# Kernel optimization log

Hardware: AMD Instinct MI355X
Metric: run time of the kernel (lower is better)

## Reference

```python
import jax, jax.numpy as jnp
import numpy as np
import math

B, QLEN, DMODEL, NHEAD, SKV = 16, 1, 2048, 32, 4096
HEAD_DIM = DMODEL // NHEAD  # 64


def setup_inputs() -> dict:
    key = jax.random.key(0)
    ks = jax.random.split(key, 12)
    x = jax.random.normal(ks[0], (B, QLEN, DMODEL), dtype=jnp.float32)
    last_pos = jax.random.randint(ks[1], (B,), 0, SKV, dtype=jnp.int64)
    # mask: attend to cache positions <= last_pos (broadcast over heads and q)
    mask = (jnp.arange(SKV)[None, :] <= last_pos[:, None]).reshape(B, 1, 1, SKV)
    s = 1.0 / math.sqrt(DMODEL)
    Wq = jax.random.normal(ks[2], (DMODEL, DMODEL), dtype=jnp.float32) * s
    bq = jax.random.normal(ks[3], (DMODEL,), dtype=jnp.float32) * 0.02
    Wk = jax.random.normal(ks[4], (DMODEL, DMODEL), dtype=jnp.float32) * s
    bk = jax.random.normal(ks[5], (DMODEL,), dtype=jnp.float32) * 0.02
    Wv = jax.random.normal(ks[6], (DMODEL, DMODEL), dtype=jnp.float32) * s
    bv = jax.random.normal(ks[7], (DMODEL,), dtype=jnp.float32) * 0.02
    Wo = jax.random.normal(ks[8], (DMODEL, DMODEL), dtype=jnp.float32) * s
    bo = jax.random.normal(ks[9], (DMODEL,), dtype=jnp.float32) * 0.02
    # prefilled KV cache (float32, as in the module)
    cache_k = jax.random.normal(ks[10], (B, NHEAD, SKV, HEAD_DIM), dtype=jnp.float32)
    cache_v = jax.random.normal(ks[11], (B, NHEAD, SKV, HEAD_DIM), dtype=jnp.float32)
    return {"x": x, "last_pos": last_pos, "mask": mask, "Wq": Wq, "bq": bq,
            "Wk": Wk, "bk": bk, "Wv": Wv, "bv": bv, "Wo": Wo, "bo": bo,
            "cache_k": cache_k, "cache_v": cache_v}


def reference(x, last_pos, mask, Wq, bq, Wk, bk, Wv, bv, Wo, bo, cache_k, cache_v):
    bsz, seq_len, _ = x.shape  # decode path: seq_len == 1
    # QKV projections -> [B, H, S, D]
    q = (x @ Wq + bq).reshape(bsz, seq_len, NHEAD, HEAD_DIM).transpose(0, 2, 1, 3)
    k = (x @ Wk + bk).reshape(bsz, seq_len, NHEAD, HEAD_DIM).transpose(0, 2, 1, 3)
    v = (x @ Wv + bv).reshape(bsz, seq_len, NHEAD, HEAD_DIM).transpose(0, 2, 1, 3)
    # KV-cache scatter update at last_pos (seq_len == 1 branch of the original)
    bidx = jnp.arange(bsz)
    updated_kcache = cache_k.at[bidx, :, last_pos, :].set(k[:, :, 0, :].astype(jnp.float32))
    updated_vcache = cache_v.at[bidx, :, last_pos, :].set(v[:, :, 0, :].astype(jnp.float32))
    kf = updated_kcache.astype(q.dtype)
    vf = updated_vcache.astype(q.dtype)
    # scores: [B, H, Q, SKV]
    scores = jnp.einsum("bhqd,bhkd->bhqk", q, kf) / math.sqrt(HEAD_DIM)
    scores = jnp.where(mask, scores, jnp.finfo(scores.dtype).min)
    probs = jax.nn.softmax(scores.astype(jnp.float32), axis=-1).astype(q.dtype)
    out = jnp.einsum("bhqk,bhkd->bhqd", probs, vf)
    out = out.transpose(0, 2, 1, 3).reshape(bsz, seq_len, -1)
    out = out @ Wo + bo
    return out, updated_kcache, updated_vcache
```

## Files before the change

### kernel.cpp

```cpp
#include <hip/hip_runtime.h>
#include <math.h>

#define BB 16
#define DMODEL 2048
#define NHEAD 32
#define SKV 4096
#define HDIM 64
#define BH (BB*NHEAD)
#define NSTRIP 16

typedef float f4 __attribute__((ext_vector_type(4)));

__global__ __launch_bounds__(256) void gemm_part(
    const float* __restrict__ src,
    const float* __restrict__ Wa, const float* __restrict__ Wb,
    const float* __restrict__ Wc,
    float* __restrict__ pa, float* __restrict__ pb, float* __restrict__ pc) {
  const float* W = (blockIdx.z == 0) ? Wa : ((blockIdx.z == 1) ? Wb : Wc);
  float* part    = (blockIdx.z == 0) ? pa : ((blockIdx.z == 1) ? pb : pc);
  __shared__ float xs[16][64];
  int tid = threadIdx.x;
  int i0 = blockIdx.y * 64;
  int o  = blockIdx.x * 1024 + tid * 4;
  {
    int t = tid * 4;
    int b = t >> 6, i = t & 63;
    *(f4*)&xs[b][i] = *(const f4*)&src[b * DMODEL + i0 + i];
  }
  __syncthreads();
  f4 acc[16];
#pragma unroll
  for (int b = 0; b < 16; ++b) acc[b] = (f4)0.f;
#pragma unroll 8
  for (int i = 0; i < 64; ++i) {
    f4 w = *(const f4*)&W[(size_t)(i0 + i) * DMODEL + o];
#pragma unroll
    for (int b = 0; b < 16; ++b) acc[b] += xs[b][i] * w;
  }
  float* p = part + (size_t)blockIdx.y * (16 * DMODEL) + o;
#pragma unroll
  for (int b = 0; b < 16; ++b) *(f4*)&p[b * DMODEL] = acc[b];
}

__global__ __launch_bounds__(256) void gemm_reduce(
    const float* __restrict__ pa, const float* __restrict__ pb,
    const float* __restrict__ pc,
    const float* __restrict__ ba, const float* __restrict__ bb,
    const float* __restrict__ bc,
    float* __restrict__ da, float* __restrict__ db, float* __restrict__ dc) {
  const float* p    = (blockIdx.y == 0) ? pa : ((blockIdx.y == 1) ? pb : pc);
  const float* bias = (blockIdx.y == 0) ? ba : ((blockIdx.y == 1) ? bb : bc);
  float* dst        = (blockIdx.y == 0) ? da : ((blockIdx.y == 1) ? db : dc);
  int idx = blockIdx.x * 256 + threadIdx.x;
  float s = bias[idx & (DMODEL - 1)];
#pragma unroll 8
  for (int t = 0; t < 32; ++t) s += p[(size_t)t * (16 * DMODEL) + idx];
  dst[idx] = s;
}

__global__ __launch_bounds__(256) void k_copy_scores(
    const float* __restrict__ cacheK, const float* __restrict__ knew,
    const float* __restrict__ qv, const int* __restrict__ last_pos,
    float* __restrict__ outK, float* __restrict__ scores,
    float* __restrict__ pstat) {
  int bh = blockIdx.x >> 4;
  int blk = blockIdx.x & 15;
  int j0 = blk << 8;
  int b = bh >> 5;
  int lp = last_pos[b];
  int tid = threadIdx.x;
  int wave = tid >> 6, lane = tid & 63, q4 = lane >> 4, l16 = lane & 15;
  int rbase = wave * 4 + q4;
  const f4 qf = ((const f4*)(qv + bh * HDIM))[l16];
  const f4 kn = ((const f4*)(knew + bh * HDIM))[l16];
  size_t base = ((size_t)bh * SKV + j0 + rbase) * 16 + l16;
  const f4* K4 = (const f4*)cacheK + base;
  f4* O4 = (f4*)outK + base;
  float* s = scores + (size_t)bh * SKV;
  float fv[16];
#pragma unroll
  for (int t = 0; t < 16; ++t) {
    int j = j0 + rbase + t * 16;
    f4 kv = __builtin_nontemporal_load(&K4[t * 256]);
    if (j == lp) kv = kn;
    __builtin_nontemporal_store(kv, &O4[t * 256]);
    float p = qf.x * kv.x + qf.y * kv.y + qf.z * kv.z + qf.w * kv.w;
    p += __shfl_xor(p, 1);
    p += __shfl_xor(p, 2);
    p += __shfl_xor(p, 4);
    p += __shfl_xor(p, 8);
    p *= 0.125f;
    bool valid = (j <= lp);
    if (l16 == 0 && valid) s[j] = p;
    fv[t] = valid ? p : -1e30f;
  }
  float m = fv[0];
#pragma unroll
  for (int t = 1; t < 16; ++t) m = fmaxf(m, fv[t]);
  m = fmaxf(m, __shfl_xor(m, 16));
  m = fmaxf(m, __shfl_xor(m, 32));
  float se = 0.f;
#pragma unroll
  for (int t = 0; t < 16; ++t) se += __expf(fv[t] - m);
  se += __shfl_xor(se, 16);
  se += __shfl_xor(se, 32);
  __shared__ float lm[4], ls[4];
  if (lane == 0) { lm[wave] = m; ls[wave] = se; }
  __syncthreads();
  if (tid == 0) {
    float M = fmaxf(fmaxf(lm[0], lm[1]), fmaxf(lm[2], lm[3]));
    float S = ls[0] * __expf(lm[0] - M) + ls[1] * __expf(lm[1] - M)
            + ls[2] * __expf(lm[2] - M) + ls[3] * __expf(lm[3] - M);
    pstat[(bh * 16 + blk) * 2 + 0] = M;
    pstat[(bh * 16 + blk) * 2 + 1] = S;
  }
}

__global__ __launch_bounds__(256) void v_copy_pv(
    const float* __restrict__ cacheV, const float* __restrict__ vnew,
    const float* __restrict__ scores, const float* __restrict__ pstat,
    const int* __restrict__ last_pos,
    float* __restrict__ outV, float* __restrict__ prec) {
  __shared__ float sm[16], ss[16], sp[256];
  __shared__ float part[4][64];
  int bh = blockIdx.x >> 4;
  int blk = blockIdx.x & 15;
  int j0 = blk << 8;
  int b = bh >> 5;
  int lp = last_pos[b];
  int tid = threadIdx.x;
  if (tid < 16) {
    sm[tid] = pstat[(bh * 16 + tid) * 2 + 0];
    ss[tid] = pstat[(bh * 16 + tid) * 2 + 1];
  }
  __syncthreads();
  float M = sm[0];
#pragma unroll
  for (int i = 1; i < 16; ++i) M = fmaxf(M, sm[i]);
  float S = 0.f;
#pragma unroll
  for (int i = 0; i < 16; ++i) S += ss[i] * __expf(sm[i] - M);
  float inv = 1.f / S;
  int jj = j0 + tid;
  sp[tid] = (jj <= lp) ? __expf(scores[(size_t)bh * SKV + jj] - M) * inv : 0.f;
  __syncthreads();

  int wave = tid >> 6, lane = tid & 63, q4 = lane >> 4, l16 = lane & 15;
  int rbase = wave * 4 + q4;
  const f4 vn = ((const f4*)(vnew + bh * HDIM))[l16];
  size_t base = ((size_t)bh * SKV + j0 + rbase) * 16 + l16;
  const f4* V4 = (const f4*)cacheV + base;
  f4* O4 = (f4*)outV + base;
  f4 acc = (f4)0.f;
#pragma unroll
  for (int t = 0; t < 16; ++t) {
    int j = j0 + rbase + t * 16;
    f4 vv = __builtin_nontemporal_load(&V4[t * 256]);
    if (j == lp) vv = vn;
    __builtin_nontemporal_store(vv, &O4[t * 256]);
    acc += sp[rbase + t * 16] * vv;
  }
  acc.x += __shfl_xor(acc.x, 16); acc.x += __shfl_xor(acc.x, 32);
  acc.y += __shfl_xor(acc.y, 16); acc.y += __shfl_xor(acc.y, 32);
  acc.z += __shfl_xor(acc.z, 16); acc.z += __shfl_xor(acc.z, 32);
  acc.w += __shfl_xor(acc.w, 16); acc.w += __shfl_xor(acc.w, 32);
  if (q4 == 0) ((f4*)part[wave])[l16] = acc;
  __syncthreads();
  if (tid < 64) {
    prec[(size_t)blockIdx.x * HDIM + tid] =
        part[0][tid] + part[1][tid] + part[2][tid] + part[3][tid];
  }
}

__global__ __launch_bounds__(256) void attn_gemm_part(
    const float* __restrict__ prec, const float* __restrict__ Wo,
    float* __restrict__ po) {
  __shared__ float xs[16][64];
  int tid = threadIdx.x;
  int h = blockIdx.y;
  {
    int g = tid >> 4, u = tid & 15;
    const float* r = prec + (size_t)(g * NHEAD + h) * NSTRIP * HDIM + u * 4;
    f4 a = (f4)0.f;
#pragma unroll
    for (int s = 0; s < 16; ++s) a += *(const f4*)&r[s * HDIM];
    *(f4*)&xs[g][u * 4] = a;
  }
  __syncthreads();
  int o = blockIdx.x * 1024 + tid * 4;
  int i0 = h * 64;
  f4 acc[16];
#pragma unroll
  for (int b = 0; b < 16; ++b) acc[b] = (f4)0.f;
#pragma unroll 8
  for (int i = 0; i < 64; ++i) {
    f4 w = *(const f4*)&Wo[(size_t)(i0 + i) * DMODEL + o];
#pragma unroll
    for (int b = 0; b < 16; ++b) acc[b] += xs[b][i] * w;
  }
  float* p = po + (size_t)blockIdx.y * (16 * DMODEL) + o;
#pragma unroll
  for (int b = 0; b < 16; ++b) *(f4*)&p[b * DMODEL] = acc[b];
}

extern "C" void kernel_launch(void* const* d_in, const int* in_sizes, int n_in,
                              void* d_out, int out_size, void* d_ws, size_t ws_size,
                              hipStream_t stream) {
  const float* x        = (const float*)d_in[0];
  const int*   last_pos = (const int*)d_in[1];
  const float* Wq = (const float*)d_in[3];
  const float* bq = (const float*)d_in[4];
  const float* Wk = (const float*)d_in[5];
  const float* bk = (const float*)d_in[6];
  const float* Wv = (const float*)d_in[7];
  const float* bv = (const float*)d_in[8];
  const float* Wo = (const float*)d_in[9];
  const float* bo = (const float*)d_in[10];
  const float* cacheK = (const float*)d_in[11];
  const float* cacheV = (const float*)d_in[12];

  float* out  = (float*)d_out;
  float* outK = out + (size_t)BB * DMODEL;
  float* outV = outK + (size_t)BH * SKV * HDIM;

  float* ws    = (float*)d_ws;
  float* q     = ws;
  float* k     = ws + 32768;
  float* v     = ws + 65536;
  float* pstat = ws + 98304;
  float* prec  = ws + 114688;
  float* big   = ws + 114688 + 524288;
  float* pq = big;
  float* pk = big + 1048576;
  float* pv = big + 2097152;
  float* scores = big;
  float* po = big + 1048576;

  gemm_part<<<dim3(2, 32, 3), 256, 0, stream>>>(x, Wq, Wk, Wv, pq, pk, pv);
  gemm_reduce<<<dim3(128, 3), 256, 0, stream>>>(pq, pk, pv, bq, bk, bv, q, k, v);
  k_copy_scores<<<8192, 256, 0, stream>>>(cacheK, k, q, last_pos, outK, scores, pstat);
  v_copy_pv<<<8192, 256, 0, stream>>>(cacheV, v, scores, pstat, last_pos, outV, prec);
  attn_gemm_part<<<dim3(2, 32), 256, 0, stream>>>(prec, Wo, po);
  gemm_reduce<<<dim3(128, 1), 256, 0, stream>>>(po, po, po, bo, bo, bo, out, out, out);
}
```

Before: 441.4 us.

## Store block-local exp scores and prefetch V before softmax stats in PV kernel

The score kernel now computes the block max first and writes unnormalized exponentials relative to that max, so the PV kernel no longer recomputes exp per element. The PV kernel issues all sixteen V-cache loads up front, before reading the stats and scores, so the memory latency overlaps with the softmax-combine work. Normalization is applied once per block through a scalar rescale factor. This adds an extra block barrier in the score kernel and more live registers in the PV kernel.

```diff
diff --git a/kernel.cpp b/kernel.cpp
--- a/kernel.cpp
+++ b/kernel.cpp
@@ -89,30 +89,31 @@
     p += __shfl_xor(p, 2);
     p += __shfl_xor(p, 4);
     p += __shfl_xor(p, 8);
-    p *= 0.125f;
-    bool valid = (j <= lp);
-    if (l16 == 0 && valid) s[j] = p;
-    fv[t] = valid ? p : -1e30f;
+    fv[t] = (j <= lp) ? p * 0.125f : -1e30f;
   }
   float m = fv[0];
 #pragma unroll
   for (int t = 1; t < 16; ++t) m = fmaxf(m, fv[t]);
   m = fmaxf(m, __shfl_xor(m, 16));
   m = fmaxf(m, __shfl_xor(m, 32));
+  __shared__ float lm[4], ls[4];
+  if (lane == 0) lm[wave] = m;
+  __syncthreads();
+  float M = fmaxf(fmaxf(lm[0], lm[1]), fmaxf(lm[2], lm[3]));
   float se = 0.f;
 #pragma unroll
-  for (int t = 0; t < 16; ++t) se += __expf(fv[t] - m);
+  for (int t = 0; t < 16; ++t) {
+    float e = __expf(fv[t] - M);
+    se += e;
+    if (l16 == 0) s[j0 + rbase + t * 16] = e;
+  }
   se += __shfl_xor(se, 16);
   se += __shfl_xor(se, 32);
-  __shared__ float lm[4], ls[4];
-  if (lane == 0) { lm[wave] = m; ls[wave] = se; }
+  if (lane == 0) ls[wave] = se;
   __syncthreads();
   if (tid == 0) {
-    float M = fmaxf(fmaxf(lm[0], lm[1]), fmaxf(lm[2], lm[3]));
-    float S = ls[0] * __expf(lm[0] - M) + ls[1] * __expf(lm[1] - M)
-            + ls[2] * __expf(lm[2] - M) + ls[3] * __expf(lm[3] - M);
     pstat[(bh * 16 + blk) * 2 + 0] = M;
-    pstat[(bh * 16 + blk) * 2 + 1] = S;
+    pstat[(bh * 16 + blk) * 2 + 1] = ls[0] + ls[1] + ls[2] + ls[3];
   }
 }
 
@@ -129,37 +130,57 @@
   int b = bh >> 5;
   int lp = last_pos[b];
   int tid = threadIdx.x;
+  int wave = tid >> 6, lane = tid & 63, q4 = lane >> 4, l16 = lane & 15;
+  int rbase = wave * 4 + q4;
+  size_t base = ((size_t)bh * SKV + j0 + rbase) * 16 + l16;
+  const f4* V4 = (const f4*)cacheV + base;
+  f4* O4 = (f4*)outV + base;
+
+  f4 v0  = __builtin_nontemporal_load(&V4[ 0 * 256]);
+  f4 v1  = __builtin_nontemporal_load(&V4[ 1 * 256]);
+  f4 v2  = __builtin_nontemporal_load(&V4[ 2 * 256]);
+  f4 v3  = __builtin_nontemporal_load(&V4[ 3 * 256]);
+  f4 v4  = __builtin_nontemporal_load(&V4[ 4 * 256]);
+  f4 v5  = __builtin_nontemporal_load(&V4[ 5 * 256]);
+  f4 v6  = __builtin_nontemporal_load(&V4[ 6 * 256]);
+  f4 v7  = __builtin_nontemporal_load(&V4[ 7 * 256]);
+  f4 v8  = __builtin_nontemporal_load(&V4[ 8 * 256]);
+  f4 v9  = __builtin_nontemporal_load(&V4[ 9 * 256]);
+  f4 v10 = __builtin_nontemporal_load(&V4[10 * 256]);
+  f4 v11 = __builtin_nontemporal_load(&V4[11 * 256]);
+  f4 v12 = __builtin_nontemporal_load(&V4[12 * 256]);
+  f4 v13 = __builtin_nontemporal_load(&V4[13 * 256]);
+  f4 v14 = __builtin_nontemporal_load(&V4[14 * 256]);
+  f4 v15 = __builtin_nontemporal_load(&V4[15 * 256]);
+  const f4 vn = ((const f4*)(vnew + bh * HDIM))[l16];
+
   if (tid < 16) {
     sm[tid] = pstat[(bh * 16 + tid) * 2 + 0];
     ss[tid] = pstat[(bh * 16 + tid) * 2 + 1];
   }
+  sp[tid] = scores[(size_t)bh * SKV + j0 + tid];
   __syncthreads();
   float M = sm[0];
 #pragma unroll
   for (int i = 1; i < 16; ++i) M = fmaxf(M, sm[i]);
-  float S = 0.f;
-#pragma unroll
-  for (int i = 0; i < 16; ++i) S += ss[i] * __expf(sm[i] - M);
-  float inv = 1.f / S;
-  int jj = j0 + tid;
-  sp[tid] = (jj <= lp) ? __expf(scores[(size_t)bh * SKV + jj] - M) * inv : 0.f;
-  __syncthreads();
-
-  int wave = tid >> 6, lane = tid & 63, q4 = lane >> 4, l16 = lane & 15;
-  int rbase = wave * 4 + q4;
-  const f4 vn = ((const f4*)(vnew + bh * HDIM))[l16];
-  size_t base = ((size_t)bh * SKV + j0 + rbase) * 16 + l16;
-  const f4* V4 = (const f4*)cacheV + base;
-  f4* O4 = (f4*)outV + base;
+  float D = 0.f;
+#pragma unroll
+  for (int i = 0; i < 16; ++i) D += ss[i] * __expf(sm[i] - M);
+  float alpha = __expf(sm[blk] - M) / D;
+
   f4 acc = (f4)0.f;
-#pragma unroll
-  for (int t = 0; t < 16; ++t) {
-    int j = j0 + rbase + t * 16;
-    f4 vv = __builtin_nontemporal_load(&V4[t * 256]);
-    if (j == lp) vv = vn;
-    __builtin_nontemporal_store(vv, &O4[t * 256]);
-    acc += sp[rbase + t * 16] * vv;
-  }
+#define STEP(t, vt)                                              \
+  {                                                              \
+    int j = j0 + rbase + t * 16;                                 \
+    if (j == lp) vt = vn;                                        \
+    __builtin_nontemporal_store(vt, &O4[t * 256]);               \
+    acc += sp[rbase + t * 16] * vt;                              \
+  }
+  STEP(0, v0)  STEP(1, v1)  STEP(2, v2)  STEP(3, v3)
+  STEP(4, v4)  STEP(5, v5)  STEP(6, v6)  STEP(7, v7)
+  STEP(8, v8)  STEP(9, v9)  STEP(10, v10) STEP(11, v11)
+  STEP(12, v12) STEP(13, v13) STEP(14, v14) STEP(15, v15)
+#undef STEP
   acc.x += __shfl_xor(acc.x, 16); acc.x += __shfl_xor(acc.x, 32);
   acc.y += __shfl_xor(acc.y, 16); acc.y += __shfl_xor(acc.y, 32);
   acc.z += __shfl_xor(acc.z, 16); acc.z += __shfl_xor(acc.z, 32);
@@ -168,7 +189,7 @@
   __syncthreads();
   if (tid < 64) {
     prec[(size_t)blockIdx.x * HDIM + tid] =
-        part[0][tid] + part[1][tid] + part[2][tid] + part[3][tid];
+        alpha * (part[0][tid] + part[1][tid] + part[2][tid] + part[3][tid]);
   }
 }
 
```

New measurement: 448.7 us. No clear change (+1.7%).
